# Optimization experiments

Hardware: AMD Instinct MI355X
Metric: run time of the kernel (lower is better)

The kernel has to match this reference:

```python
import jax, jax.numpy as jnp
import numpy as np

# config constants (init_kwargs)
WC, WS = 0.5, 0.5            # boundary cosine / structural weights (hybrid mode)
TARGET_BPP = 6.0             # target_bytes_per_patch
GAIN = 1.0                   # target_patch_gain
THRESH = 0.5                 # boundary_threshold; mask = p >= THRESH
EPS = 1e-6

_POP6 = jnp.array([bin(i).count('1') for i in range(64)], dtype=jnp.int32)

def _pop6(x):
    return _POP6[jnp.clip(x, 0, 63)]

def _logit(p):
    p = jnp.clip(p, EPS, 1.0 - EPS)
    return jnp.log(p) - jnp.log1p(-p)

def _next(x):  # shift-left by one, zero-padded at end (matches torch q_next pattern)
    return jnp.concatenate([x[1:], jnp.zeros((1,), x.dtype)])

def _hist(vals, mask, bins):
    idx = jnp.where(mask, vals, bins)  # invalid -> out of range, dropped
    return jnp.zeros((bins,), jnp.int32).at[idx].add(1, mode='drop')


def setup_inputs() -> dict:
    key = jax.random.key(0)
    ks = jax.random.split(key, 6)
    B, S = 4, 1048576
    return {
        'boundary_logprobs': jax.random.normal(ks[0], (B, S), jnp.float32),
        'states': jax.random.randint(ks[1], (B, S), 0, 4096, jnp.int32),
        'q_class': jax.random.randint(ks[2], (B, S), 0, 64, jnp.int32),
        'family': jax.random.randint(ks[3], (B, S), 0, 4, jnp.int32),
        'micro_ref': jax.random.randint(ks[4], (B, S), 0, 64, jnp.int32),
        'valid_mask': jax.random.randint(ks[5], (B, S), 0, 2, jnp.int32).astype(bool),
    }


def reference(boundary_logprobs, states, q_class, family, micro_ref, valid_mask):
    B, S = valid_mask.shape
    v = valid_mask.reshape(-1)
    st = states.reshape(-1).astype(jnp.int32)
    q = q_class.reshape(-1).astype(jnp.int32)
    fam = family.reshape(-1).astype(jnp.int32)
    mic = micro_ref.reshape(-1).astype(jnp.int32)

    # --- structural boundary probs ---
    omega12 = st & 0xFFF
    c6 = ((omega12 >> 6) ^ omega12) & 63          # chirality6
    d_chi = jnp.clip(_pop6(c6 ^ _next(c6)).astype(jnp.float32) / 6.0, 0.0, 1.0)
    d_q = _pop6((q & 63) ^ (_next(q) & 63)).astype(jnp.float32) / 6.0
    fx = (fam & 3) ^ (_next(fam) & 3)
    d_fam = (((fx & 1) != 0).astype(jnp.float32) + ((fx & 2) != 0).astype(jnp.float32)) / 2.0
    score = jnp.clip(0.5 * d_chi + 0.35 * d_q + 0.15 * d_fam, EPS, 1.0)
    structural = jnp.where(v, score, 0.0)

    # --- combine with cosine probs (hybrid mode) ---
    cosine = jnp.exp(jnp.minimum(boundary_logprobs.reshape(-1), 0.0))
    combined = (WC * cosine + WS * structural) / max(WC + WS, 1e-6)

    # --- target bytes-per-patch rate adjustment ---
    vf = v.astype(jnp.float32)
    vc = jnp.maximum(jnp.sum(vf), 1.0)
    cur = jnp.clip(jnp.sum(combined * vf) / vc, 1e-4, 1.0 - 1e-4)
    tgt = max(1e-4, min(1.0 - 1e-4, 1.0 / TARGET_BPP))
    shift = _logit(jnp.asarray(tgt, jnp.float32)) - _logit(cur)
    combined = jax.nn.sigmoid(_logit(combined) + GAIN * shift)
    combined = jnp.clip(combined, EPS, 1.0 - EPS)
    combined_logprobs = jnp.log(combined)
    bmask = combined_logprobs >= jnp.log(jnp.asarray(THRESH, jnp.float32))

    # --- histograms over effective (valid) positions ---
    shell = _pop6(c6)
    q_hist64 = _hist(q, v, 64)
    family_hist4 = _hist(fam, v, 4)
    micro_hist64 = _hist(mic, v, 64)
    shell_hist7 = _hist(shell, v, 7)
    wt_q = _pop6(q & 63)
    q_weight_hist7 = _hist(wt_q, v, 7)
    bits = ((q & 63)[:, None] >> jnp.arange(6)) & 1            # [n, 6]
    bit_excitation6 = jnp.sum(bits * v[:, None].astype(jnp.int32), axis=0)

    # --- patch lengths (vectorized run-length over valid bytes) ---
    bv = bmask & v
    pos = jnp.cumsum(v.astype(jnp.int32))                      # 1-indexed valid position
    bpos = jnp.where(bv, pos, 0)
    prev = jax.lax.cummax(jnp.concatenate([jnp.zeros((1,), jnp.int32), bpos[:-1]]))
    lengths = jnp.where(bv, pos - prev, 0)                     # dense run lengths at boundaries
    total_valid = pos[-1]
    trailing = total_valid - jax.lax.cummax(bpos)[-1]          # open trailing run
    patch_count = jnp.sum(bv).astype(jnp.int32) + (trailing > 0).astype(jnp.int32)

    return (combined_logprobs.reshape(B, S), bmask.reshape(B, S), structural.reshape(B, S),
            q_hist64, family_hist4, micro_hist64, shell_hist7, q_weight_hist7,
            bit_excitation6, lengths, trailing, patch_count)
```

## Files before the change

kernel.cpp:

```cpp
#include <hip/hip_runtime.h>

#define TPB 256
#define EPT 8
#define CHUNK (TPB * EPT)
#define P2T 1024
#define NSLICE 64

typedef unsigned long long ull;

__device__ __forceinline__ ull shfl_down_u64(ull x, int off) {
    unsigned lo = (unsigned)x, hi = (unsigned)(x >> 32);
    lo = __shfl_down(lo, off, 64);
    hi = __shfl_down(hi, off, 64);
    return ((ull)hi << 32) | lo;
}

__global__ __launch_bounds__(TPB, 4) void k_pass1(
    const float* __restrict__ blp, const int* __restrict__ st,
    const int* __restrict__ q, const int* __restrict__ fam,
    const int* __restrict__ mic, const int* __restrict__ vm,
    float* __restrict__ out_structural,
    int* __restrict__ blocksum_v, double* __restrict__ blocksum_c,
    int* __restrict__ ghist, int n)
{
    __shared__ int lh2[2048];
    __shared__ int slhs[11];
    __shared__ int swv[4];
    __shared__ float swc[4];

    const int tid = threadIdx.x, lane = tid & 63, wave = tid >> 6;
    const long i0 = (long)blockIdx.x * CHUNK + (long)tid * EPT;
    const bool fast = ((long)(blockIdx.x + 1) * CHUNK <= n);

    int stv[9], qv[9], fv[9], micv[8], vmv[8];
    float bpv[8];
    if (fast) {
        const int4 sa = *(const int4*)(st + i0),  sb = *(const int4*)(st + i0 + 4);
        const int4 qa = *(const int4*)(q + i0),   qb = *(const int4*)(q + i0 + 4);
        const int4 fa = *(const int4*)(fam + i0), fb = *(const int4*)(fam + i0 + 4);
        const int4 ma = *(const int4*)(mic + i0), mb = *(const int4*)(mic + i0 + 4);
        const int4 va = *(const int4*)(vm + i0),  vb = *(const int4*)(vm + i0 + 4);
        const float4 ba = *(const float4*)(blp + i0), bb = *(const float4*)(blp + i0 + 4);
        int nst = __shfl_down(sa.x, 1, 64);
        int nq  = __shfl_down(qa.x, 1, 64);
        int nf  = __shfl_down(fa.x, 1, 64);
        if (lane == 63) {
            const long j = i0 + 8;
            nst = (j < n) ? st[j]  : 0;
            nq  = (j < n) ? q[j]   : 0;
            nf  = (j < n) ? fam[j] : 0;
        }
        stv[0]=sa.x; stv[1]=sa.y; stv[2]=sa.z; stv[3]=sa.w; stv[4]=sb.x; stv[5]=sb.y; stv[6]=sb.z; stv[7]=sb.w; stv[8]=nst;
        qv[0]=qa.x;  qv[1]=qa.y;  qv[2]=qa.z;  qv[3]=qa.w;  qv[4]=qb.x;  qv[5]=qb.y;  qv[6]=qb.z;  qv[7]=qb.w;  qv[8]=nq;
        fv[0]=fa.x;  fv[1]=fa.y;  fv[2]=fa.z;  fv[3]=fa.w;  fv[4]=fb.x;  fv[5]=fb.y;  fv[6]=fb.z;  fv[7]=fb.w;  fv[8]=nf;
        micv[0]=ma.x; micv[1]=ma.y; micv[2]=ma.z; micv[3]=ma.w; micv[4]=mb.x; micv[5]=mb.y; micv[6]=mb.z; micv[7]=mb.w;
        vmv[0]=va.x; vmv[1]=va.y; vmv[2]=va.z; vmv[3]=va.w; vmv[4]=vb.x; vmv[5]=vb.y; vmv[6]=vb.z; vmv[7]=vb.w;
        bpv[0]=ba.x; bpv[1]=ba.y; bpv[2]=ba.z; bpv[3]=ba.w; bpv[4]=bb.x; bpv[5]=bb.y; bpv[6]=bb.z; bpv[7]=bb.w;
    } else {
        #pragma unroll
        for (int e = 0; e < 8; ++e) {
            long ii = i0 + e;
            bool r = ii < n;
            stv[e] = r ? st[ii] : 0;  qv[e] = r ? q[ii] : 0;  fv[e] = r ? fam[ii] : 0;
            micv[e] = r ? mic[ii] : 0; vmv[e] = r ? vm[ii] : 0; bpv[e] = r ? blp[ii] : 0.f;
        }
        stv[8] = (i0 + 8 < n) ? st[i0 + 8] : 0;
        qv[8]  = (i0 + 8 < n) ? q[i0 + 8] : 0;
        fv[8]  = (i0 + 8 < n) ? fam[i0 + 8] : 0;
    }

    for (int t = tid; t < 2048; t += TPB) lh2[t] = 0;
    if (tid < 11) slhs[tid] = 0;
    __syncthreads();

    const int qrow = ((wave << 2) | (lane & 3)) << 6;
    int sv = 0;
    float scf = 0.0f;
    ull accF = 0, accS0 = 0, accS1 = 0;
    float structural[8];
    #pragma unroll
    for (int e = 0; e < 8; ++e) {
        int sti = stv[e], qi = qv[e], fi = fv[e], mi = micv[e];
        int v = (vmv[e] != 0);
        int om  = sti & 0xFFF;      int c6  = ((om  >> 6) ^ om ) & 63;
        int omn = stv[e+1] & 0xFFF; int c6n = ((omn >> 6) ^ omn) & 63;
        float d_chi = (float)__popc(c6 ^ c6n) * (1.0f / 6.0f);
        float d_q   = (float)__popc((qi & 63) ^ (qv[e+1] & 63)) * (1.0f / 6.0f);
        int fx = (fi & 3) ^ (fv[e+1] & 3);
        float d_fam = (float)((fx & 1) + ((fx >> 1) & 1)) * 0.5f;
        float score = 0.5f * d_chi + 0.35f * d_q + 0.15f * d_fam;
        score = fminf(fmaxf(score, 1e-6f), 1.0f);
        structural[e] = v ? score : 0.0f;
        float cosine = expf(fminf(bpv[e], 0.0f));
        float combined = 0.5f * (cosine + structural[e]);
        if (v) {
            sv += 1;
            scf += combined;
            atomicAdd(&lh2[qrow + (qi & 63)], 1);
            atomicAdd(&lh2[1024 + qrow + (mi & 63)], 1);
            accF += 1ULL << ((fi & 3) * 16);
            int sh = __popc(c6);
            ull ts = 1ULL << ((sh & 3) * 16);
            if (sh < 4) accS0 += ts; else accS1 += ts;
        }
    }

    if (fast) {
        float4 o;
        o.x=structural[0]; o.y=structural[1]; o.z=structural[2]; o.w=structural[3];
        *(float4*)(out_structural + i0) = o;
        o.x=structural[4]; o.y=structural[5]; o.z=structural[6]; o.w=structural[7];
        *(float4*)(out_structural + i0 + 4) = o;
    } else {
        #pragma unroll
        for (int e = 0; e < 8; ++e)
            if (i0 + e < n) out_structural[i0 + e] = structural[e];
    }

    #pragma unroll
    for (int off = 32; off > 0; off >>= 1) {
        sv  += __shfl_down(sv, off, 64);
        scf += __shfl_down(scf, off, 64);
        accF  += shfl_down_u64(accF, off);
        accS0 += shfl_down_u64(accS0, off);
        accS1 += shfl_down_u64(accS1, off);
    }
    if (lane == 0) {
        swv[wave] = sv; swc[wave] = scf;
        #pragma unroll
        for (int b2 = 0; b2 < 4; ++b2) atomicAdd(&slhs[b2],     (int)((accF  >> (16*b2)) & 0xFFFF));
        #pragma unroll
        for (int b2 = 0; b2 < 4; ++b2) atomicAdd(&slhs[4 + b2], (int)((accS0 >> (16*b2)) & 0xFFFF));
        #pragma unroll
        for (int b2 = 0; b2 < 3; ++b2) atomicAdd(&slhs[8 + b2], (int)((accS1 >> (16*b2)) & 0xFFFF));
    }
    __syncthreads();
    if (tid == 0) {
        blocksum_v[blockIdx.x] = swv[0] + swv[1] + swv[2] + swv[3];
        blocksum_c[blockIdx.x] = (double)swc[0] + (double)swc[1] + (double)swc[2] + (double)swc[3];
    }
    int* gh = ghist + (blockIdx.x & (NSLICE - 1)) * 152;
    for (int t2 = tid; t2 < 139; t2 += TPB) {
        int val;
        if (t2 < 64) {
            val = 0;
            #pragma unroll
            for (int r = 0; r < 16; ++r) val += lh2[(r << 6) + t2];
        } else if (t2 < 68) {
            val = slhs[t2 - 64];
        } else if (t2 < 132) {
            int b2 = t2 - 68;
            val = 0;
            #pragma unroll
            for (int r = 0; r < 16; ++r) val += lh2[1024 + (r << 6) + b2];
        } else {
            val = slhs[4 + (t2 - 132)];
        }
        if (val) atomicAdd(&gh[t2], val);
    }
}

__global__ __launch_bounds__(P2T) void k_pass2(
    const int* __restrict__ bsv, const double* __restrict__ bsc, int nb,
    int* __restrict__ pos_offset, float* __restrict__ shiftp,
    int* __restrict__ totalv_p, const int* __restrict__ ghist,
    float* __restrict__ out_hist)
{
    __shared__ int s[P2T];
    __shared__ double d[P2T];
    __shared__ int qh[64];
    int t = threadIdx.x;
    int c0 = 2 * t, c1 = 2 * t + 1;
    int v0 = (c0 < nb) ? bsv[c0] : 0;
    int v1 = (c1 < nb) ? bsv[c1] : 0;
    double x0 = (c0 < nb) ? bsc[c0] : 0.0;
    double x1 = (c1 < nb) ? bsc[c1] : 0.0;
    s[t] = v0 + v1; d[t] = x0 + x1;
    if (t < 139) {
        int acc = 0;
        #pragma unroll 8
        for (int sl = 0; sl < NSLICE; ++sl) acc += ghist[sl * 152 + t];
        out_hist[t] = (float)acc;
        if (t < 64) qh[t] = acc;
    }
    __syncthreads();
    for (int off = 1; off < P2T; off <<= 1) {
        int add = (t >= off) ? s[t - off] : 0;
        __syncthreads();
        s[t] += add;
        __syncthreads();
    }
    if (c0 < nb) pos_offset[c0] = s[t] - v0 - v1;
    if (c1 < nb) pos_offset[c1] = s[t] - v1;
    for (int off = P2T / 2; off > 0; off >>= 1) {
        if (t < off) d[t] += d[t + off];
        __syncthreads();
    }
    if (t == 0) {
        int total_v = s[P2T - 1];
        *totalv_p = total_v;
        double vc = (double)(total_v > 1 ? total_v : 1);
        float cur = (float)(d[0] / vc);
        cur = fminf(fmaxf(cur, 1e-4f), 0.9999f);
        float p = fminf(fmaxf(cur, 1e-6f), 0.999999f);
        float lc = logf(p) - log1pf(-p);
        float tgt = (float)(1.0 / 6.0);
        float lt = logf(tgt) - log1pf(-tgt);
        *shiftp = lt - lc;
    }
    if (t < 7) {
        int sacc = 0;
        for (int b = 0; b < 64; ++b) if (__popc(b) == t) sacc += qh[b];
        out_hist[139 + t] = (float)sacc;
    }
    if (t < 6) {
        int sacc = 0;
        for (int b = 0; b < 64; ++b) sacc += qh[b] * ((b >> t) & 1);
        out_hist[146 + t] = (float)sacc;
    }
}

__global__ __launch_bounds__(TPB, 8) void k_pass3(
    const float* __restrict__ strc, const float* __restrict__ blp,
    const float* __restrict__ shiftp, const int* __restrict__ pos_offset,
    float* __restrict__ out_logp, float* __restrict__ out_bmask,
    float* __restrict__ out_len, int* __restrict__ chunk_cnt,
    int* __restrict__ chunk_last, ull* __restrict__ chunk_first, int n)
{
    __shared__ int swt[4], swm[4], scnt[4];
    __shared__ ull sfirst[4];
    const int tid = threadIdx.x, lane = tid & 63, wave = tid >> 6;
    const long i0 = (long)blockIdx.x * CHUNK + (long)tid * EPT;
    const bool fast = ((long)(blockIdx.x + 1) * CHUNK <= n);
    const float shift = *shiftp;

    float sv8[8], bp8[8];
    if (fast) {
        const float4 s0 = *(const float4*)(strc + i0), s1 = *(const float4*)(strc + i0 + 4);
        const float4 p0 = *(const float4*)(blp + i0),  p1 = *(const float4*)(blp + i0 + 4);
        sv8[0]=s0.x; sv8[1]=s0.y; sv8[2]=s0.z; sv8[3]=s0.w; sv8[4]=s1.x; sv8[5]=s1.y; sv8[6]=s1.z; sv8[7]=s1.w;
        bp8[0]=p0.x; bp8[1]=p0.y; bp8[2]=p0.z; bp8[3]=p0.w; bp8[4]=p1.x; bp8[5]=p1.y; bp8[6]=p1.z; bp8[7]=p1.w;
    } else {
        #pragma unroll
        for (int e = 0; e < 8; ++e) {
            long ii = i0 + e;
            bool r = ii < n;
            sv8[e] = r ? strc[ii] : 0.0f;
            bp8[e] = r ? blp[ii] : 0.0f;
        }
    }

    unsigned mv = 0, mb = 0;
    float lp[8], bmf[8], lenv[8];
    #pragma unroll
    for (int e = 0; e < 8; ++e) {
        float s = sv8[e];
        int v = (s > 0.0f);
        float cosine = expf(fminf(bp8[e], 0.0f));
        float comb = 0.5f * (cosine + s);
        float p = fminf(fmaxf(comb, 1e-6f), 0.999999f);
        float z = logf(p) - log1pf(-p) + shift;
        float sgm = 1.0f / (1.0f + expf(-z));
        sgm = fminf(fmaxf(sgm, 1e-6f), 0.999999f);
        float clp = logf(sgm);
        lp[e] = clp;
        int bm = (clp >= -0.69314718f) ? 1 : 0;
        bmf[e] = (float)bm;
        mv |= (unsigned)v << e;
        if (bm & v) mb |= 1u << e;
        lenv[e] = 0.0f;
    }
    if (fast) {
        float4 o;
        o.x=lp[0]; o.y=lp[1]; o.z=lp[2]; o.w=lp[3];     *(float4*)(out_logp + i0) = o;
        o.x=lp[4]; o.y=lp[5]; o.z=lp[6]; o.w=lp[7];     *(float4*)(out_logp + i0 + 4) = o;
        o.x=bmf[0]; o.y=bmf[1]; o.z=bmf[2]; o.w=bmf[3]; *(float4*)(out_bmask + i0) = o;
        o.x=bmf[4]; o.y=bmf[5]; o.z=bmf[6]; o.w=bmf[7]; *(float4*)(out_bmask + i0 + 4) = o;
    } else {
        #pragma unroll
        for (int e = 0; e < 8; ++e)
            if (i0 + e < n) { out_logp[i0 + e] = lp[e]; out_bmask[i0 + e] = bmf[e]; }
    }

    int tvc = __popc(mv);
    int x = tvc;
    #pragma unroll
    for (int off = 1; off < 64; off <<= 1) {
        int y = __shfl_up(x, off, 64);
        if (lane >= off) x += y;
    }
    if (lane == 63) swt[wave] = x;
    __syncthreads();
    int wb = pos_offset[blockIdx.x];
    for (int w2 = 0; w2 < wave; ++w2) wb += swt[w2];
    const int vbase = wb + (x - tvc);

    int last = -1;
    if (mb) {
        int hb = 31 - __clz(mb);
        last = vbase + __popc(mv & ((2u << hb) - 1));
    }
    int m = last;
    #pragma unroll
    for (int off = 1; off < 64; off <<= 1) {
        int y = __shfl_up(m, off, 64);
        if (lane >= off && y > m) m = y;
    }
    int exm = __shfl_up(m, 1, 64);
    if (lane == 0) exm = -1;
    if (lane == 63) swm[wave] = m;
    int cnt = __popc(mb);
    ull fp = ~0ULL;
    if (mb) {
        int lb = __ffs(mb) - 1;
        int fv2 = vbase + __popc(mv & ((2u << lb) - 1));
        fp = ((ull)(unsigned)(i0 + lb) << 32) | (unsigned)fv2;
    }
    #pragma unroll
    for (int off = 32; off > 0; off >>= 1) {
        cnt += __shfl_down(cnt, off, 64);
        ull fo = shfl_down_u64(fp, off);
        if (fo < fp) fp = fo;
    }
    if (lane == 0) { scnt[wave] = cnt; sfirst[wave] = fp; }
    __syncthreads();

    int prev = exm;
    for (int w2 = 0; w2 < wave; ++w2) if (swm[w2] > prev) prev = swm[w2];
    int runv = 0;
    #pragma unroll
    for (int e = 0; e < 8; ++e) {
        runv += (mv >> e) & 1;
        if ((mb >> e) & 1) {
            int pos = vbase + runv;
            lenv[e] = (prev >= 0) ? (float)(pos - prev) : 0.0f;
            prev = pos;
        }
    }
    if (fast) {
        float4 o;
        o.x=lenv[0]; o.y=lenv[1]; o.z=lenv[2]; o.w=lenv[3]; *(float4*)(out_len + i0) = o;
        o.x=lenv[4]; o.y=lenv[5]; o.z=lenv[6]; o.w=lenv[7]; *(float4*)(out_len + i0 + 4) = o;
    } else {
        #pragma unroll
        for (int e = 0; e < 8; ++e)
            if (i0 + e < n) out_len[i0 + e] = lenv[e];
    }
    if (tid == 0) {
        int c = scnt[0] + scnt[1] + scnt[2] + scnt[3];
        int L = swm[0];
        if (swm[1] > L) L = swm[1];
        if (swm[2] > L) L = swm[2];
        if (swm[3] > L) L = swm[3];
        ull F = sfirst[0];
        if (sfirst[1] < F) F = sfirst[1];
        if (sfirst[2] < F) F = sfirst[2];
        if (sfirst[3] < F) F = sfirst[3];
        chunk_cnt[blockIdx.x] = c;
        chunk_last[blockIdx.x] = L > 0 ? L : 0;
        chunk_first[blockIdx.x] = F;
    }
}

__global__ __launch_bounds__(P2T) void k_pass4(
    const int* __restrict__ chunk_cnt, const int* __restrict__ chunk_last,
    const ull* __restrict__ chunk_first, const int* __restrict__ totalv_p,
    int nb, float* __restrict__ out_len,
    float* __restrict__ out_trailing, float* __restrict__ out_patch)
{
    __shared__ int s[P2T];
    __shared__ int cs[P2T];
    int t = threadIdx.x;
    int c0 = 2 * t, c1 = 2 * t + 1;
    int a = 0, b = 0;
    if (c0 < nb) { int z = chunk_last[c0]; a = z > 0 ? z : 0; }
    if (c1 < nb) { int z = chunk_last[c1]; b = z > 0 ? z : 0; }
    int cnt = ((c0 < nb) ? chunk_cnt[c0] : 0) + ((c1 < nb) ? chunk_cnt[c1] : 0);
    s[t] = a > b ? a : b;
    cs[t] = cnt;
    __syncthreads();
    for (int off = 1; off < P2T; off <<= 1) {
        int y = (t >= off) ? s[t - off] : 0;
        __syncthreads();
        if (y > s[t]) s[t] = y;
        __syncthreads();
    }
    int excl = (t > 0) ? s[t - 1] : 0;
    int carry0 = excl;
    int carry1 = excl > a ? excl : a;
    if (c0 < nb) {
        ull F = chunk_first[c0];
        if (F != ~0ULL) {
            int fi = (int)(F >> 32);
            int fv2 = (int)(F & 0xFFFFFFFFu);
            out_len[fi] = (float)(fv2 - carry0);
        }
    }
    if (c1 < nb) {
        ull F = chunk_first[c1];
        if (F != ~0ULL) {
            int fi = (int)(F >> 32);
            int fv2 = (int)(F & 0xFFFFFFFFu);
            out_len[fi] = (float)(fv2 - carry1);
        }
    }
    int gmax = s[P2T - 1];
    __syncthreads();
    for (int off = P2T / 2; off > 0; off >>= 1) {
        if (t < off) cs[t] += cs[t + off];
        __syncthreads();
    }
    if (t == 0) {
        int total_v = *totalv_p;
        int trailing = total_v - gmax;
        int patch = cs[0] + (trailing > 0 ? 1 : 0);
        *out_trailing = (float)trailing;
        *out_patch = (float)patch;
    }
}

extern "C" void kernel_launch(void* const* d_in, const int* in_sizes, int n_in,
                              void* d_out, int out_size, void* d_ws, size_t ws_size,
                              hipStream_t stream)
{
    const float* blp = (const float*)d_in[0];
    const int* st   = (const int*)d_in[1];
    const int* q    = (const int*)d_in[2];
    const int* fam  = (const int*)d_in[3];
    const int* mic  = (const int*)d_in[4];
    const int* vm   = (const int*)d_in[5];
    const int n = in_sizes[0];
    const int nb = (n + CHUNK - 1) / CHUNK;

    float* out = (float*)d_out;
    float* out_logp       = out;
    float* out_bmask      = out + (size_t)n;
    float* out_structural = out + 2 * (size_t)n;
    float* out_hist       = out + 3 * (size_t)n;
    float* out_len        = out + 3 * (size_t)n + 152;
    float* out_trailing   = out + 4 * (size_t)n + 152;
    float* out_patch      = out + 4 * (size_t)n + 153;

    char* w = (char*)d_ws;
    int*    ghist      = (int*)(w);
    int*    blocksum_v = (int*)(w + 40960);
    int*    pos_offset = (int*)(w + 57344);
    int*    chunk_cnt  = (int*)(w + 73728);
    int*    chunk_last = (int*)(w + 90112);
    float*  shiftp     = (float*)(w + 106496);
    int*    totalv_p   = (int*)(w + 106500);
    double* blocksum_c = (double*)(w + 110592);
    ull*    chunk_first= (ull*)(w + 131072);

    hipMemsetAsync(ghist, 0, NSLICE * 152 * 4, stream);

    k_pass1<<<dim3(nb), dim3(TPB), 0, stream>>>(
        blp, st, q, fam, mic, vm, out_structural,
        blocksum_v, blocksum_c, ghist, n);

    k_pass2<<<dim3(1), dim3(P2T), 0, stream>>>(
        blocksum_v, blocksum_c, nb, pos_offset, shiftp, totalv_p,
        ghist, out_hist);

    k_pass3<<<dim3(nb), dim3(TPB), 0, stream>>>(
        out_structural, blp, shiftp, pos_offset, out_logp, out_bmask,
        out_len, chunk_cnt, chunk_last, chunk_first, n);

    k_pass4<<<dim3(1), dim3(P2T), 0, stream>>>(
        chunk_cnt, chunk_last, chunk_first, totalv_p, nb, out_len,
        out_trailing, out_patch);
}
```

Before: 193.3 us.

## Fold single-block scan pass into pass3 via redundant per-block prefix sums

Removes the single-block k_pass2 launch. Each k_pass3 block now reads all per-block sums itself to compute its own prefix offset, the total valid count and the logit shift, and block 0 reduces the histograms. This trades a serial one-block kernel and its launch gap for redundant reads of about 2048 block sums per block. The change also raises k_pass1 occupancy to 8 blocks and zeroes shared histogram memory with vector int4 stores.

```diff
diff --git a/kernel.cpp b/kernel.cpp
--- a/kernel.cpp
+++ b/kernel.cpp
@@ -15,7 +15,7 @@
     return ((ull)hi << 32) | lo;
 }
 
-__global__ __launch_bounds__(TPB, 4) void k_pass1(
+__global__ __launch_bounds__(TPB, 8) void k_pass1(
     const float* __restrict__ blp, const int* __restrict__ st,
     const int* __restrict__ q, const int* __restrict__ fam,
     const int* __restrict__ mic, const int* __restrict__ vm,
@@ -69,7 +69,11 @@
         fv[8]  = (i0 + 8 < n) ? fam[i0 + 8] : 0;
     }
 
-    for (int t = tid; t < 2048; t += TPB) lh2[t] = 0;
+    {
+        int4 z4; z4.x = 0; z4.y = 0; z4.z = 0; z4.w = 0;
+        *(int4*)&lh2[tid * 8] = z4;
+        *(int4*)&lh2[tid * 8 + 4] = z4;
+    }
     if (tid < 11) slhs[tid] = 0;
     __syncthreads();
 
@@ -160,79 +164,24 @@
     }
 }
 
-__global__ __launch_bounds__(P2T) void k_pass2(
-    const int* __restrict__ bsv, const double* __restrict__ bsc, int nb,
-    int* __restrict__ pos_offset, float* __restrict__ shiftp,
-    int* __restrict__ totalv_p, const int* __restrict__ ghist,
-    float* __restrict__ out_hist)
-{
-    __shared__ int s[P2T];
-    __shared__ double d[P2T];
-    __shared__ int qh[64];
-    int t = threadIdx.x;
-    int c0 = 2 * t, c1 = 2 * t + 1;
-    int v0 = (c0 < nb) ? bsv[c0] : 0;
-    int v1 = (c1 < nb) ? bsv[c1] : 0;
-    double x0 = (c0 < nb) ? bsc[c0] : 0.0;
-    double x1 = (c1 < nb) ? bsc[c1] : 0.0;
-    s[t] = v0 + v1; d[t] = x0 + x1;
-    if (t < 139) {
-        int acc = 0;
-        #pragma unroll 8
-        for (int sl = 0; sl < NSLICE; ++sl) acc += ghist[sl * 152 + t];
-        out_hist[t] = (float)acc;
-        if (t < 64) qh[t] = acc;
-    }
-    __syncthreads();
-    for (int off = 1; off < P2T; off <<= 1) {
-        int add = (t >= off) ? s[t - off] : 0;
-        __syncthreads();
-        s[t] += add;
-        __syncthreads();
-    }
-    if (c0 < nb) pos_offset[c0] = s[t] - v0 - v1;
-    if (c1 < nb) pos_offset[c1] = s[t] - v1;
-    for (int off = P2T / 2; off > 0; off >>= 1) {
-        if (t < off) d[t] += d[t + off];
-        __syncthreads();
-    }
-    if (t == 0) {
-        int total_v = s[P2T - 1];
-        *totalv_p = total_v;
-        double vc = (double)(total_v > 1 ? total_v : 1);
-        float cur = (float)(d[0] / vc);
-        cur = fminf(fmaxf(cur, 1e-4f), 0.9999f);
-        float p = fminf(fmaxf(cur, 1e-6f), 0.999999f);
-        float lc = logf(p) - log1pf(-p);
-        float tgt = (float)(1.0 / 6.0);
-        float lt = logf(tgt) - log1pf(-tgt);
-        *shiftp = lt - lc;
-    }
-    if (t < 7) {
-        int sacc = 0;
-        for (int b = 0; b < 64; ++b) if (__popc(b) == t) sacc += qh[b];
-        out_hist[139 + t] = (float)sacc;
-    }
-    if (t < 6) {
-        int sacc = 0;
-        for (int b = 0; b < 64; ++b) sacc += qh[b] * ((b >> t) & 1);
-        out_hist[146 + t] = (float)sacc;
-    }
-}
-
 __global__ __launch_bounds__(TPB, 8) void k_pass3(
     const float* __restrict__ strc, const float* __restrict__ blp,
-    const float* __restrict__ shiftp, const int* __restrict__ pos_offset,
+    const int* __restrict__ bsv, const double* __restrict__ bsc,
+    const int* __restrict__ ghist,
     float* __restrict__ out_logp, float* __restrict__ out_bmask,
     float* __restrict__ out_len, int* __restrict__ chunk_cnt,
-    int* __restrict__ chunk_last, ull* __restrict__ chunk_first, int n)
+    int* __restrict__ chunk_last, ull* __restrict__ chunk_first,
+    int* __restrict__ totalv_p, float* __restrict__ out_hist, int n)
 {
     __shared__ int swt[4], swm[4], scnt[4];
     __shared__ ull sfirst[4];
+    __shared__ int sB[4], sT[4];
+    __shared__ double sC[4];
+    __shared__ int qh[64];
     const int tid = threadIdx.x, lane = tid & 63, wave = tid >> 6;
     const long i0 = (long)blockIdx.x * CHUNK + (long)tid * EPT;
     const bool fast = ((long)(blockIdx.x + 1) * CHUNK <= n);
-    const float shift = *shiftp;
+    const int nb = (int)gridDim.x;
 
     float sv8[8], bp8[8];
     if (fast) {
@@ -248,6 +197,37 @@
             sv8[e] = r ? strc[ii] : 0.0f;
             bp8[e] = r ? blp[ii] : 0.0f;
         }
+    }
+
+    int bsum = 0, tsum = 0;
+    double csum = 0.0;
+    for (int c = tid; c < nb; c += TPB) {
+        int vv = bsv[c];
+        tsum += vv;
+        if (c < (int)blockIdx.x) bsum += vv;
+        csum += bsc[c];
+    }
+    #pragma unroll
+    for (int off = 32; off > 0; off >>= 1) {
+        bsum += __shfl_down(bsum, off, 64);
+        tsum += __shfl_down(tsum, off, 64);
+        csum += __shfl_down(csum, off, 64);
+    }
+    if (lane == 0) { sB[wave] = bsum; sT[wave] = tsum; sC[wave] = csum; }
+    __syncthreads();
+    const int wb0     = sB[0] + sB[1] + sB[2] + sB[3];
+    const int total_v = sT[0] + sT[1] + sT[2] + sT[3];
+    const double dtot = sC[0] + sC[1] + sC[2] + sC[3];
+    float shift;
+    {
+        double vc = (double)(total_v > 1 ? total_v : 1);
+        float cur = (float)(dtot / vc);
+        cur = fminf(fmaxf(cur, 1e-4f), 0.9999f);
+        float p = fminf(fmaxf(cur, 1e-6f), 0.999999f);
+        float lc = logf(p) - log1pf(-p);
+        float tgt = (float)(1.0 / 6.0);
+        float lt = logf(tgt) - log1pf(-tgt);
+        shift = lt - lc;
     }
 
     unsigned mv = 0, mb = 0;
@@ -291,7 +271,7 @@
     }
     if (lane == 63) swt[wave] = x;
     __syncthreads();
-    int wb = pos_offset[blockIdx.x];
+    int wb = wb0;
     for (int w2 = 0; w2 < wave; ++w2) wb += swt[w2];
     const int vbase = wb + (x - tvc);
 
@@ -359,6 +339,28 @@
         chunk_cnt[blockIdx.x] = c;
         chunk_last[blockIdx.x] = L > 0 ? L : 0;
         chunk_first[blockIdx.x] = F;
+    }
+
+    if (blockIdx.x == 0) {
+        if (tid < 139) {
+            int acc = 0;
+            #pragma unroll 8
+            for (int sl = 0; sl < NSLICE; ++sl) acc += ghist[sl * 152 + tid];
+            out_hist[tid] = (float)acc;
+            if (tid < 64) qh[tid] = acc;
+        }
+        if (tid == 0) *totalv_p = total_v;
+        __syncthreads();
+        if (tid < 7) {
+            int sacc = 0;
+            for (int b = 0; b < 64; ++b) if (__popc(b) == tid) sacc += qh[b];
+            out_hist[139 + tid] = (float)sacc;
+        }
+        if (tid < 6) {
+            int sacc = 0;
+            for (int b = 0; b < 64; ++b) sacc += qh[b] * ((b >> tid) & 1);
+            out_hist[146 + tid] = (float)sacc;
+        }
     }
 }
 
@@ -444,10 +446,8 @@
     char* w = (char*)d_ws;
     int*    ghist      = (int*)(w);
     int*    blocksum_v = (int*)(w + 40960);
-    int*    pos_offset = (int*)(w + 57344);
     int*    chunk_cnt  = (int*)(w + 73728);
     int*    chunk_last = (int*)(w + 90112);
-    float*  shiftp     = (float*)(w + 106496);
     int*    totalv_p   = (int*)(w + 106500);
     double* blocksum_c = (double*)(w + 110592);
     ull*    chunk_first= (ull*)(w + 131072);
@@ -458,13 +458,10 @@
         blp, st, q, fam, mic, vm, out_structural,
         blocksum_v, blocksum_c, ghist, n);
 
-    k_pass2<<<dim3(1), dim3(P2T), 0, stream>>>(
-        blocksum_v, blocksum_c, nb, pos_offset, shiftp, totalv_p,
-        ghist, out_hist);
-
     k_pass3<<<dim3(nb), dim3(TPB), 0, stream>>>(
-        out_structural, blp, shiftp, pos_offset, out_logp, out_bmask,
-        out_len, chunk_cnt, chunk_last, chunk_first, n);
+        out_structural, blp, blocksum_v, blocksum_c, ghist,
+        out_logp, out_bmask, out_len, chunk_cnt, chunk_last, chunk_first,
+        totalv_p, out_hist, n);
 
     k_pass4<<<dim3(1), dim3(P2T), 0, stream>>>(
         chunk_cnt, chunk_last, chunk_first, totalv_p, nb, out_len,
```

Measured after the change: 193.1 us. Within noise of the previous version (-0.1%).
